# Kernel tuning notes

Hardware: AMD Instinct MI355X
Metric: run time of the kernel (lower is better)

## Reference

```python
import jax, jax.numpy as jnp
import numpy as np

D_MODEL = 2048
D_INNER = 4096            # expand * d_model
D_XB = 1024
D_STATE = 128
HEADDIM = 64
NHEADS = D_INNER // HEADDIM            # 64
NGROUPS = D_INNER // D_STATE           # 32 (d_inner == ngroups * d_state)
HPG = NHEADS // NGROUPS                # heads per B/C group = 2
REPEAT = D_INNER // D_XB               # repeat_kv factor = 4
XB_GROUPS = D_XB // D_STATE            # 8
CHUNK = 256
D_CONV = 4
CONV_DIM = D_INNER + 2 * D_XB          # 6144
D_IN_PROJ = D_INNER + 2 * D_XB + D_INNER + NHEADS  # 10304 -> d_mlp = 0
NORM_GS = D_INNER // NGROUPS           # gated group-RMSNorm group size = 128
EPS = 1e-5


def setup_inputs() -> dict:
    key = jax.random.key(0)
    ks = jax.random.split(key, 8)
    u = jax.random.normal(ks[0], (2, 2048, D_MODEL), jnp.float32)
    W_in = jax.random.normal(ks[1], (D_IN_PROJ, D_MODEL), jnp.float32) * 0.02
    conv_w = jax.random.normal(ks[2], (CONV_DIM, D_CONV), jnp.float32) * 0.2
    conv_b = jnp.zeros((CONV_DIM,), jnp.float32)
    # dt_bias = inverse-softplus of dt ~ LogUniform(dt_min, dt_max), as in __init__
    dt = jnp.exp(jax.random.uniform(ks[3], (NHEADS,), jnp.float32)
                 * (np.log(0.1) - np.log(0.001)) + np.log(0.001))
    dt_bias = dt + jnp.log(-jnp.expm1(-dt))
    A_log = jnp.log(jax.random.uniform(ks[4], (NHEADS,), jnp.float32, minval=1.0, maxval=16.0))
    D = jnp.ones((NHEADS,), jnp.float32)
    norm_weight = jnp.ones((D_INNER,), jnp.float32)
    W_out = jax.random.normal(ks[5], (D_MODEL, D_INNER), jnp.float32) * 0.02
    return dict(u=u, W_in=W_in, conv_w=conv_w, conv_b=conv_b, dt_bias=dt_bias,
                A_log=A_log, D=D, norm_weight=norm_weight, W_out=W_out)


def _segsum(x):
    # x: (..., T); out[..., t, s] = sum_{s < i <= t} x_i for s <= t else -inf
    T = x.shape[-1]
    cs = jnp.cumsum(x, axis=-1)
    seg = cs[..., :, None] - cs[..., None, :]
    mask = jnp.tril(jnp.ones((T, T), bool))
    return jnp.where(mask, seg, -jnp.inf)


def _chunked_scan(x, dt, A, Bh, Ch, D):
    # SSD chunked selective scan (mamba_chunk_scan_combined math).
    # x: (b,l,h,p), dt: (b,l,h) post-softplus, A: (h,), Bh/Ch: (b,l,h,n), D: (h,)
    b, l, h, p = x.shape
    c = l // CHUNK
    xc = x.reshape(b, c, CHUNK, h, p)
    dtc = dt.reshape(b, c, CHUNK, h)
    Bc = Bh.reshape(b, c, CHUNK, h, D_STATE)
    Cc = Ch.reshape(b, c, CHUNK, h, D_STATE)
    dA = jnp.transpose(dtc * A, (0, 3, 1, 2))          # (b,h,c,cl)
    dA_cs = jnp.cumsum(dA, axis=-1)                     # (b,h,c,cl)
    L = jnp.exp(_segsum(dA))                            # (b,h,c,cl,cl), lower-tri decay
    xdt = xc * dtc[..., None]                           # (b,c,cl,h,p)
    # intra-chunk (diagonal block) output
    G = jnp.einsum('bclhn,bcshn->bhcls', Cc, Bc)
    Y_diag = jnp.einsum('bhcls,bcshp->bclhp', G * L, xdt)
    # per-chunk final states
    decay_states = jnp.exp(dA_cs[..., -1:] - dA_cs)     # (b,h,c,cl)
    states = jnp.einsum('bcshn,bhcs,bcshp->bchpn', Bc, decay_states, xdt)
    # inter-chunk recurrence
    chunk_decay = jnp.exp(dA_cs[..., -1])               # (b,h,c)
    states_t = jnp.moveaxis(states, 1, 0)               # (c,b,h,p,n)
    decay_t = jnp.moveaxis(chunk_decay, -1, 0)          # (c,b,h)
    def step(carry, inp):
        s, d = inp
        return carry * d[..., None, None] + s, carry
    _, prev = jax.lax.scan(step, jnp.zeros_like(states_t[0]), (states_t, decay_t))
    prev = jnp.moveaxis(prev, 0, 1)                     # (b,c,h,p,n) state entering each chunk
    Y_off = jnp.einsum('bclhn,bchpn,bhcl->bclhp', Cc, prev, jnp.exp(dA_cs))
    y = Y_diag + Y_off + xc * D[:, None]                # D skip uses raw x
    return y.reshape(b, l, h, p)


def reference(u, W_in, conv_w, conv_b, dt_bias, A_log, D, norm_weight, W_out):
    b, l, _ = u.shape
    zxbcdt = u @ W_in.T                                 # (b,l,10304); d_mlp == 0
    z, xBC, dt = jnp.split(zxbcdt, [D_INNER, D_INNER + CONV_DIM], axis=-1)
    # causal depthwise conv1d (kernel D_CONV) + SiLU (causal_conv1d_fn semantics)
    xp = jnp.pad(xBC, ((0, 0), (D_CONV - 1, 0), (0, 0)))
    conv = conv_b
    for k in range(D_CONV):
        conv = conv + xp[:, k:k + l, :] * conv_w[:, k]
    xBC = jax.nn.silu(conv)
    x, B, C = jnp.split(xBC, [D_XB, 2 * D_XB], axis=-1)
    # GQA-style repeat_kv (repeat_interleave over d_state-sized groups)
    x = jnp.repeat(x.reshape(b, l, XB_GROUPS, D_STATE), REPEAT, axis=2).reshape(b, l, D_INNER)
    B = jnp.repeat(B.reshape(b, l, XB_GROUPS, D_STATE), REPEAT, axis=2)   # (b,l,NGROUPS,n)
    C = C.reshape(b, l, NGROUPS, D_STATE)
    # broadcast groups to heads (head h uses group h // HPG)
    Bh = jnp.repeat(B, HPG, axis=2)
    Ch = jnp.repeat(C, HPG, axis=2)
    xh = x.reshape(b, l, NHEADS, HEADDIM)
    dt = jax.nn.softplus(dt + dt_bias)                  # dt_softplus=True
    A = -jnp.exp(A_log)
    y = _chunked_scan(xh, dt, A, Bh, Ch, D).reshape(b, l, D_INNER)
    # RMSNormGated (norm_before_gate=False): gate then grouped RMSNorm
    y = y * jax.nn.silu(z)
    yg = y.reshape(b, l, NGROUPS, NORM_GS)
    rstd = jax.lax.rsqrt(jnp.mean(yg * yg, axis=-1, keepdims=True) + EPS)
    y = (yg * rstd).reshape(b, l, D_INNER) * norm_weight
    return y @ W_out.T
```

## Files before the change

kernel.cpp:

```cpp
#include <hip/hip_runtime.h>
#include <cstdint>
#include <cstddef>

typedef unsigned int uint;
typedef unsigned short ushort;

typedef __bf16 bf16x8 __attribute__((ext_vector_type(8)));
typedef float f32x4 __attribute__((ext_vector_type(4)));

__device__ __forceinline__ float bflo(uint u) { return __uint_as_float(u << 16); }
__device__ __forceinline__ float bfhi(uint u) { return __uint_as_float(u & 0xffff0000u); }
__device__ __forceinline__ float bf2f(ushort s) { return __uint_as_float(((uint)s) << 16); }
__device__ __forceinline__ ushort f2bf(float f) {
    uint u = __float_as_uint(f);
    u += 0x7fffu + ((u >> 16) & 1u);
    return (ushort)(u >> 16);
}
__device__ __forceinline__ uint pk2(float lo, float hi) {
    return (uint)f2bf(lo) | ((uint)f2bf(hi) << 16);
}
__device__ __forceinline__ void unpack8(uint4 v, float* f) {
    f[0] = bflo(v.x); f[1] = bfhi(v.x); f[2] = bflo(v.y); f[3] = bfhi(v.y);
    f[4] = bflo(v.z); f[5] = bfhi(v.z); f[6] = bflo(v.w); f[7] = bfhi(v.w);
}

typedef __attribute__((address_space(1))) const unsigned int* as1_cuptr;
typedef __attribute__((address_space(3))) unsigned int* as3_uptr;
__device__ __forceinline__ void gload_lds16(const void* g, void* l) {
    __builtin_amdgcn_global_load_lds((as1_cuptr)g, (as3_uptr)l, 16, 0, 0);
}

#define LTOT 4096
#define DMODEL 2048
#define DINNER 4096
#define DSTATE 128
#define NHEADS 64
#define CONVDIM 6144
#define DPROJ 10304
#define CHUNK 256
#define NCHUNK 16

__global__ void cvt_kernel(const float* __restrict__ in, ushort* __restrict__ out, int n4) {
    int i = blockIdx.x * 256 + threadIdx.x;
    if (i < n4) {
        float4 v = ((const float4*)in)[i];
        ushort4 o;
        o.x = f2bf(v.x); o.y = f2bf(v.y); o.z = f2bf(v.z); o.w = f2bf(v.w);
        ((ushort4*)out)[i] = o;
    }
}

#define MFMA_OP __builtin_amdgcn_mfma_f32_16x16x32_bf16
#define MMX(MB, AV, BV) do { \
  _Pragma("unroll") \
  for (int _m = 0; _m < 4; _m++) \
    _Pragma("unroll") \
    for (int _n = 0; _n < 4; _n++) \
      acc[(MB)+_m][_n] = MFMA_OP(AV[_m], BV[_n], acc[(MB)+_m][_n], 0, 0, 0); \
} while (0)

#define RD8(BASE, OFF) (*(const bf16x8*)((BASE) + (OFF)))

__global__ __launch_bounds__(512, 2) void gemm256_in(
    const ushort* __restrict__ X, const ushort* __restrict__ W,
    ushort* __restrict__ zbuf, ushort* __restrict__ xbc, float* __restrict__ dtraw) {
    __shared__ ushort AL[2][16384];
    __shared__ ushort BL[2][16384];
    const int NBN = 41;
    int q = gridDim.x >> 3;
    int wg = blockIdx.x;
    int swz = (wg & 7) * q + (wg >> 3);
    int per = NBN * 4;
    int sg = swz / per, rr = swz % per;
    int bm = sg * 4 + (rr & 3);
    int bn = rr >> 2;
    int tid = threadIdx.x;
    int lane = tid & 63, w = tid >> 6;
    int wr = w >> 2, wc = w & 3;
    int lr = lane & 15, g = lane >> 4;
    int y00 = ((lr >> 1) << 7) | ((lr & 1) << 6) | (g << 4);
    int z00 = y00 ^ (((y00 >> 7) & 7) << 4);
    int aBase = wr * 8192 + z00;
    int bBase = wc * 4096 + z00;
    int z0 = tid * 16, z1 = z0 + 8192;
    int y0 = z0 ^ (((z0 >> 7) & 7) << 4);
    int y1 = z1 ^ (((z1 >> 7) & 7) << 4);
    int row0s = ((y0 >> 7) << 1) | ((y0 >> 6) & 1), kbe0 = (y0 & 63) >> 1;
    int row1s = ((y1 >> 7) << 1) | ((y1 >> 6) & 1), kbe1 = (y1 & 63) >> 1;
    const ushort* gA0 = &X[(size_t)(bm * 256 + row0s) * 2048 + kbe0];
    const ushort* gA1 = &X[(size_t)(bm * 256 + row1s) * 2048 + kbe1];
    const ushort* gB0 = &W[(size_t)(bn * 256 + row0s) * 2048 + kbe0];
    const ushort* gB1 = &W[(size_t)(bn * 256 + row1s) * 2048 + kbe1];
    int wOff = w * 1024;

#define STAGE(DB, ARR, KP, P0, P1, KO) do { \
    gload_lds16((P0) + (KO) + (KP) * 32, (char*)(ARR) + (DB) * 32768 + (KP) * 16384 + wOff); \
    gload_lds16((P1) + (KO) + (KP) * 32, (char*)(ARR) + (DB) * 32768 + (KP) * 16384 + wOff + 8192); \
} while (0)

    f32x4 acc[8][4] = {};
    bf16x8 bLo[4], bHi[4], aE[4], aO[4];
    STAGE(0, AL, 0, gA0, gA1, 0);
    STAGE(0, BL, 0, gB0, gB1, 0);
    STAGE(0, AL, 1, gA0, gA1, 0);
    STAGE(0, BL, 1, gB0, gB1, 0);
    asm volatile("s_waitcnt vmcnt(4)" ::: "memory");
    __builtin_amdgcn_s_barrier();
    __builtin_amdgcn_sched_barrier(0);
    {
        const char* Ab = (const char*)AL;
        const char* Bb = (const char*)BL;
        #pragma unroll
        for (int i = 0; i < 4; i++) {
            bLo[i] = RD8(Bb, bBase + i * 1024);
            aE[i]  = RD8(Ab, aBase + i * 1024);
        }
    }

    for (int t = 0; t < 32; ++t) {
        int buf = t & 1, nb = buf ^ 1;
        int ko = ((t + 1) & 31) * 64;
        const char* Ab  = (const char*)AL + buf * 32768;
        const char* Bb  = (const char*)BL + buf * 32768;
        const char* AbN = (const char*)AL + nb * 32768;
        const char* BbN = (const char*)BL + nb * 32768;
        #pragma unroll
        for (int i = 0; i < 4; i++) aO[i] = RD8(Ab, aBase + 4096 + i * 1024);
        STAGE(nb, AL, 0, gA0, gA1, ko);
        __builtin_amdgcn_s_setprio(1);
        MMX(0, aE, bLo);
        __builtin_amdgcn_s_setprio(0);
        __builtin_amdgcn_sched_barrier(0);
        asm volatile("s_waitcnt vmcnt(2)" ::: "memory");
        __builtin_amdgcn_s_barrier();
        __builtin_amdgcn_sched_barrier(0);
        #pragma unroll
        for (int i = 0; i < 4; i++) {
            bHi[i] = RD8(Bb, bBase + 16384 + i * 1024);
            aE[i]  = RD8(Ab, aBase + 16384 + i * 1024);
        }
        STAGE(nb, BL, 0, gB0, gB1, ko);
        __builtin_amdgcn_s_setprio(1);
        MMX(4, aO, bLo);
        __builtin_amdgcn_s_setprio(0);
        __builtin_amdgcn_sched_barrier(0);
        #pragma unroll
        for (int i = 0; i < 4; i++) aO[i] = RD8(Ab, aBase + 16384 + 4096 + i * 1024);
        STAGE(nb, AL, 1, gA0, gA1, ko);
        __builtin_amdgcn_s_setprio(1);
        MMX(0, aE, bHi);
        __builtin_amdgcn_s_setprio(0);
        __builtin_amdgcn_sched_barrier(0);
        asm volatile("s_waitcnt vmcnt(2)" ::: "memory");
        __builtin_amdgcn_s_barrier();
        __builtin_amdgcn_sched_barrier(0);
        #pragma unroll
        for (int i = 0; i < 4; i++) {
            bLo[i] = RD8(BbN, bBase + i * 1024);
            aE[i]  = RD8(AbN, aBase + i * 1024);
        }
        STAGE(nb, BL, 1, gB0, gB1, ko);
        __builtin_amdgcn_s_setprio(1);
        MMX(4, aO, bHi);
        __builtin_amdgcn_s_setprio(0);
        __builtin_amdgcn_sched_barrier(0);
    }
    asm volatile("s_waitcnt vmcnt(0)" ::: "memory");

    int rq = g * 4;
    #pragma unroll
    for (int mf = 0; mf < 8; mf++) {
        int row0 = bm * 256 + wr * 128 + mf * 16 + rq;
        #pragma unroll
        for (int n = 0; n < 4; n++) {
            int cb0 = bn * 256 + wc * 64 + n * 16;
            int col = cb0 + lr;
            if (cb0 < 4096) {
                #pragma unroll
                for (int r = 0; r < 4; r++)
                    zbuf[(size_t)(row0 + r) * DINNER + col] = f2bf(acc[mf][n][r]);
            } else if (cb0 < 10240) {
                #pragma unroll
                for (int r = 0; r < 4; r++)
                    xbc[(size_t)(row0 + r) * CONVDIM + (col - 4096)] = f2bf(acc[mf][n][r]);
            } else if (cb0 < 10304) {
                #pragma unroll
                for (int r = 0; r < 4; r++)
                    dtraw[(size_t)(row0 + r) * 64 + (col - 10240)] = acc[mf][n][r];
            }
        }
    }
}
#undef STAGE

#define MM16(MB) do { \
  acc[(MB)+0][0]=MFMA_OP(a0,b0,acc[(MB)+0][0],0,0,0); acc[(MB)+0][1]=MFMA_OP(a0,b1,acc[(MB)+0][1],0,0,0); \
  acc[(MB)+0][2]=MFMA_OP(a0,b2,acc[(MB)+0][2],0,0,0); acc[(MB)+0][3]=MFMA_OP(a0,b3,acc[(MB)+0][3],0,0,0); \
  acc[(MB)+1][0]=MFMA_OP(a1,b0,acc[(MB)+1][0],0,0,0); acc[(MB)+1][1]=MFMA_OP(a1,b1,acc[(MB)+1][1],0,0,0); \
  acc[(MB)+1][2]=MFMA_OP(a1,b2,acc[(MB)+1][2],0,0,0); acc[(MB)+1][3]=MFMA_OP(a1,b3,acc[(MB)+1][3],0,0,0); \
  acc[(MB)+2][0]=MFMA_OP(a2,b0,acc[(MB)+2][0],0,0,0); acc[(MB)+2][1]=MFMA_OP(a2,b1,acc[(MB)+2][1],0,0,0); \
  acc[(MB)+2][2]=MFMA_OP(a2,b2,acc[(MB)+2][2],0,0,0); acc[(MB)+2][3]=MFMA_OP(a2,b3,acc[(MB)+2][3],0,0,0); \
  acc[(MB)+3][0]=MFMA_OP(a3,b0,acc[(MB)+3][0],0,0,0); acc[(MB)+3][1]=MFMA_OP(a3,b1,acc[(MB)+3][1],0,0,0); \
  acc[(MB)+3][2]=MFMA_OP(a3,b2,acc[(MB)+3][2],0,0,0); acc[(MB)+3][3]=MFMA_OP(a3,b3,acc[(MB)+3][3],0,0,0); \
} while (0)

__global__ __launch_bounds__(512, 2) void gemm256_out(
    const ushort* __restrict__ X, const ushort* __restrict__ W,
    float* __restrict__ outF) {
    __shared__ ushort AL[2][16384];
    __shared__ ushort BL[2][8192];
    int q = gridDim.x >> 3;
    int wg = blockIdx.x;
    int swz = (wg & 7) * q + (wg >> 3);
    int per = 16 * 4;
    int sg = swz / per, rr = swz % per;
    int bm = sg * 4 + (rr & 3);
    int bn = rr >> 2;
    int tid = threadIdx.x;
    int lane = tid & 63, w = tid >> 6;
    int wr = w >> 1, wc = w & 1;
    int lr = lane & 15, g = lane >> 4;
    int y00 = ((lr >> 1) << 7) | ((lr & 1) << 6) | (g << 4);
    int z00 = y00 ^ (((y00 >> 7) & 7) << 4);
    int aBase = wr * 4096 + z00;
    int bBase = wc * 4096 + z00;
    int z0 = tid * 16, z1 = z0 + 8192;
    int y0 = z0 ^ (((z0 >> 7) & 7) << 4);
    int y1 = z1 ^ (((z1 >> 7) & 7) << 4);
    int rowA0 = ((y0 >> 7) << 1) | ((y0 >> 6) & 1), kA0 = (y0 & 63) >> 1;
    int rowA1 = ((y1 >> 7) << 1) | ((y1 >> 6) & 1), kA1 = (y1 & 63) >> 1;
    const ushort* gA0 = &X[(size_t)(bm * 256 + rowA0) * 4096 + kA0];
    const ushort* gA1 = &X[(size_t)(bm * 256 + rowA1) * 4096 + kA1];
    const ushort* gB  = &W[(size_t)(bn * 128 + rowA0) * 4096 + kA0];
    int wOff = w * 1024;

#define STAGEA(DB, KP, KO) do { \
    gload_lds16(gA0 + (KO) + (KP) * 32, (char*)AL + (DB) * 32768 + (KP) * 16384 + wOff); \
    gload_lds16(gA1 + (KO) + (KP) * 32, (char*)AL + (DB) * 32768 + (KP) * 16384 + wOff + 8192); \
} while (0)
#define STAGEB(DB, KP, KO) \
    gload_lds16(gB + (KO) + (KP) * 32, (char*)BL + (DB) * 16384 + (KP) * 8192 + wOff)

    f32x4 acc[4][4] = {};
    STAGEA(0, 0, 0); STAGEB(0, 0, 0);
    STAGEA(0, 1, 0); STAGEB(0, 1, 0);

    for (int t = 0; t < 64; ++t) {
        int buf = t & 1, nb = buf ^ 1;
        int ko = ((t + 1) & 63) * 64;
        const char* Ab = (const char*)AL + buf * 32768;
        const char* Bb = (const char*)BL + buf * 16384;
        bf16x8 a0, a1, a2, a3, b0, b1, b2, b3;
        asm volatile("s_waitcnt vmcnt(3)" ::: "memory");
        __builtin_amdgcn_s_barrier();
        __builtin_amdgcn_sched_barrier(0);
        b0 = RD8(Bb, bBase);        b1 = RD8(Bb, bBase + 1024);
        b2 = RD8(Bb, bBase + 2048); b3 = RD8(Bb, bBase + 3072);
        a0 = RD8(Ab, aBase);        a1 = RD8(Ab, aBase + 1024);
        a2 = RD8(Ab, aBase + 2048); a3 = RD8(Ab, aBase + 3072);
        STAGEA(nb, 0, ko); STAGEB(nb, 0, ko);
        __builtin_amdgcn_s_setprio(1);
        MM16(0);
        __builtin_amdgcn_s_setprio(0);
        __builtin_amdgcn_sched_barrier(0);
        asm volatile("s_waitcnt vmcnt(3)" ::: "memory");
        __builtin_amdgcn_s_barrier();
        __builtin_amdgcn_sched_barrier(0);
        b0 = RD8(Bb, bBase + 8192);        b1 = RD8(Bb, bBase + 8192 + 1024);
        b2 = RD8(Bb, bBase + 8192 + 2048); b3 = RD8(Bb, bBase + 8192 + 3072);
        a0 = RD8(Ab, aBase + 16384);        a1 = RD8(Ab, aBase + 16384 + 1024);
        a2 = RD8(Ab, aBase + 16384 + 2048); a3 = RD8(Ab, aBase + 16384 + 3072);
        STAGEA(nb, 1, ko); STAGEB(nb, 1, ko);
        __builtin_amdgcn_s_setprio(1);
        MM16(0);
        __builtin_amdgcn_s_setprio(0);
        __builtin_amdgcn_sched_barrier(0);
    }
    asm volatile("s_waitcnt vmcnt(0)" ::: "memory");

    int rq = g * 4;
    #pragma unroll
    for (int mf = 0; mf < 4; mf++) {
        int row0 = bm * 256 + wr * 64 + mf * 16 + rq;
        #pragma unroll
        for (int nf = 0; nf < 4; nf++) {
            int col = bn * 128 + wc * 64 + nf * 16 + lr;
            #pragma unroll
            for (int r = 0; r < 4; r++)
                outF[(size_t)(row0 + r) * DMODEL + col] = acc[mf][nf][r];
        }
    }
}
#undef STAGEA
#undef STAGEB

__global__ void conv_kernel(const ushort* __restrict__ xbc, const float* __restrict__ cw,
                            const float* __restrict__ cb, ushort* __restrict__ convout) {
    int c8 = (blockIdx.x * 256 + threadIdx.x) * 8;
    int row0 = blockIdx.y * 4;
    int t0 = row0 & 2047;
    float bias[8];
    {
        float4 b0 = ((const float4*)cb)[c8 / 4];
        float4 b1 = ((const float4*)cb)[c8 / 4 + 1];
        bias[0] = b0.x; bias[1] = b0.y; bias[2] = b0.z; bias[3] = b0.w;
        bias[4] = b1.x; bias[5] = b1.y; bias[6] = b1.z; bias[7] = b1.w;
    }
    float wk[8][4];
    #pragma unroll
    for (int e = 0; e < 8; e++) {
        float4 wv = ((const float4*)cw)[c8 + e];
        wk[e][0] = wv.x; wk[e][1] = wv.y; wk[e][2] = wv.z; wk[e][3] = wv.w;
    }
    float f[7][8];
    #pragma unroll
    for (int j = 0; j < 7; j++) {
        int tt = t0 - 3 + j;
        if (tt >= 0) {
            uint4 v = *(const uint4*)&xbc[(size_t)(row0 - 3 + j) * CONVDIM + c8];
            unpack8(v, f[j]);
        } else {
            #pragma unroll
            for (int e = 0; e < 8; e++) f[j][e] = 0.f;
        }
    }
    #pragma unroll
    for (int r = 0; r < 4; r++) {
        float a[8];
        #pragma unroll
        for (int e = 0; e < 8; e++) {
            a[e] = bias[e];
            #pragma unroll
            for (int k = 0; k < 4; k++) a[e] += f[r + k][e] * wk[e][k];
        }
        uint4 o;
        float s[8];
        #pragma unroll
        for (int e = 0; e < 8; e++) s[e] = a[e] / (1.f + __expf(-a[e]));
        o.x = pk2(s[0], s[1]); o.y = pk2(s[2], s[3]);
        o.z = pk2(s[4], s[5]); o.w = pk2(s[6], s[7]);
        *(uint4*)&convout[(size_t)(row0 + r) * CONVDIM + c8] = o;
    }
}

__global__ void cumsum_kernel(float* __restrict__ dtbuf, const float* __restrict__ dt_bias,
                              const float* __restrict__ A_log, float* __restrict__ dAcs) {
    int bi = blockIdx.x;
    int h = bi & 63, cg = bi >> 6;
    int t = threadIdx.x;
    size_t didx = (size_t)(cg * 256 + t) * 64 + h;
    float x = dtbuf[didx] + dt_bias[h];
    float sp = (x > 20.f) ? x : log1pf(__expf(x));
    dtbuf[didx] = sp;
    float A = -expf(A_log[h]);
    float v = sp * A;
    __shared__ float s[256];
    s[t] = v;
    __syncthreads();
    for (int off = 1; off < 256; off <<= 1) {
        float add = (t >= off) ? s[t - off] : 0.f;
        __syncthreads();
        s[t] += add;
        __syncthreads();
    }
    dAcs[(size_t)bi * 256 + t] = s[t];
}

__global__ __launch_bounds__(256) void states_mfma(
    const ushort* __restrict__ convout, const float* __restrict__ dtsp,
    const float* __restrict__ dAcs, float* __restrict__ states) {
    __shared__ ushort BT[128 * 72];
    __shared__ ushort XT[64 * 72];
    int bi = blockIdx.x;
    int h = bi & 63, cg = bi >> 6;
    int tid = threadIdx.x;
    int rowbase = cg * 256;
    int bcol = 1024 + ((h >> 3) << 7);
    int xcol = ((h >> 3) << 7) + ((h & 1) << 6);
    float dAlast = dAcs[(size_t)bi * 256 + 255];
    int w = tid >> 6, lane = tid & 63, g = lane >> 4, cc = lane & 15;
    f32x4 acc[4][2] = {};
    for (int T = 0; T < 4; T++) {
        __syncthreads();
        int s = lane;
        int srow = rowbase + T * 64 + s;
        #pragma unroll
        for (int i = 0; i < 4; i++) {
            int n0 = (w + i * 4) * 8;
            uint4 v = *(const uint4*)&convout[(size_t)srow * CONVDIM + bcol + n0];
            ushort us[8];
            us[0] = (ushort)v.x; us[1] = (ushort)(v.x >> 16);
            us[2] = (ushort)v.y; us[3] = (ushort)(v.y >> 16);
            us[4] = (ushort)v.z; us[5] = (ushort)(v.z >> 16);
            us[6] = (ushort)v.w; us[7] = (ushort)(v.w >> 16);
            #pragma unroll
            for (int e = 0; e < 8; e++) BT[(n0 + e) * 72 + s] = us[e];
        }
        float wgt = dtsp[(size_t)srow * 64 + h] * __expf(dAlast - dAcs[(size_t)bi * 256 + T * 64 + s]);
        #pragma unroll
        for (int j = 0; j < 2; j++) {
            int p0 = (w * 2 + j) * 8;
            uint4 v = *(const uint4*)&convout[(size_t)srow * CONVDIM + xcol + p0];
            float f[8]; unpack8(v, f);
            #pragma unroll
            for (int e = 0; e < 8; e++) XT[(p0 + e) * 72 + s] = f2bf(f[e] * wgt);
        }
        __syncthreads();
        bf16x8 af[4][2], bw[2][2];
        #pragma unroll
        for (int m = 0; m < 4; m++)
            #pragma unroll
            for (int kb = 0; kb < 2; kb++)
                af[m][kb] = *(const bf16x8*)&XT[(m * 16 + cc) * 72 + kb * 32 + 8 * g];
        #pragma unroll
        for (int np = 0; np < 2; np++)
            #pragma unroll
            for (int kb = 0; kb < 2; kb++)
                bw[np][kb] = *(const bf16x8*)&BT[(w * 32 + np * 16 + cc) * 72 + kb * 32 + 8 * g];
        #pragma unroll
        for (int m = 0; m < 4; m++)
            #pragma unroll
            for (int np = 0; np < 2; np++) {
                acc[m][np] = MFMA_OP(af[m][0], bw[np][0], acc[m][np], 0, 0, 0);
                acc[m][np] = MFMA_OP(af[m][1], bw[np][1], acc[m][np], 0, 0, 0);
            }
    }
    size_t base = (size_t)bi * 8192;
    #pragma unroll
    for (int m = 0; m < 4; m++)
        #pragma unroll
        for (int np = 0; np < 2; np++)
            #pragma unroll
            for (int r = 0; r < 4; r++) {
                int p = m * 16 + 4 * g + r;
                int n = w * 32 + np * 16 + cc;
                states[base + (size_t)p * 128 + n] = acc[m][np][r];
            }
}

__global__ void recur_kernel(const float* __restrict__ dAcs, float* __restrict__ states) {
    int blk = blockIdx.x;
    int pq = blk & 7, bh = blk >> 3;
    int h = bh & 63, b = bh >> 6;
    int tid = threadIdx.x;
    int p = pq * 8 + (tid >> 5);
    int n0 = (tid & 31) * 4;
    float4 carry = make_float4(0.f, 0.f, 0.f, 0.f);
    for (int c = 0; c < 8; c++) {
        int bi = (b * 8 + c) * 64 + h;
        float decay = __expf(dAcs[(size_t)bi * 256 + 255]);
        size_t idx = (size_t)bi * 8192 + (size_t)p * 128 + n0;
        float4 tmp = *(const float4*)&states[idx];
        *(float4*)&states[idx] = carry;
        carry.x = carry.x * decay + tmp.x;
        carry.y = carry.y * decay + tmp.y;
        carry.z = carry.z * decay + tmp.z;
        carry.w = carry.w * decay + tmp.w;
    }
}

__global__ __launch_bounds__(256, 2) void yscan_mfma(
    const ushort* __restrict__ convout, const float* __restrict__ dtsp,
    const float* __restrict__ dAcs, const float* __restrict__ states,
    ushort* __restrict__ y) {
    __shared__ ushort XT[64 * 264];
    __shared__ ushort PR[64 * 136];
    __shared__ ushort PV[4 * 16 * 72];
    __shared__ float sdA[256];
    int bi = blockIdx.x;
    int h = bi & 63, cg = bi >> 6;
    int tid = threadIdx.x;
    int rowbase = cg * 256;
    int bcol = 1024 + ((h >> 3) << 7);
    int ccol = 2048 + ((h >> 1) << 7);
    int xcol = ((h >> 3) << 7) + ((h & 1) << 6);

    sdA[tid] = dAcs[(size_t)bi * 256 + tid];
    #pragma unroll
    for (int i = 0; i < 4; i++) {
        int s = i * 64 + (tid & 63);
        float dtv = dtsp[(size_t)(rowbase + s) * 64 + h];
        #pragma unroll
        for (int j = 0; j < 2; j++) {
            int p0 = (((tid >> 6) << 1) + j) << 3;
            uint4 v = *(const uint4*)&convout[(size_t)(rowbase + s) * CONVDIM + xcol + p0];
            float f[8]; unpack8(v, f);
            #pragma unroll
            for (int e = 0; e < 8; e++) XT[(p0 + e) * 264 + s] = f2bf(f[e] * dtv);
        }
    }
    {
        const float* pv = &states[(size_t)bi * 8192];
        #pragma unroll
        for (int i = 0; i < 8; i++) {
            int flat = i * 1024 + tid * 4;
            float4 v = *(const float4*)&pv[flat];
            int p = flat >> 7, n = flat & 127;
            *(uint*)&PR[p * 136 + n]     = pk2(v.x, v.y);
            *(uint*)&PR[p * 136 + n + 2] = pk2(v.z, v.w);
        }
    }
    __syncthreads();

    int w = tid >> 6, lane = tid & 63, g = lane >> 4, c = lane & 15;
    int wbase = w * 64;
    const ushort* Crow0 = &convout[(size_t)(rowbase + wbase + c) * CONVDIM + ccol + 8 * g];

    f32x4 yac[4][4] = {};
    #pragma unroll
    for (int kb = 0; kb < 4; kb++) {
        bf16x8 pb[4];
        #pragma unroll
        for (int np = 0; np < 4; np++)
            pb[np] = *(const bf16x8*)&PR[(16 * np + c) * 136 + kb * 32 + 8 * g];
        #pragma unroll
        for (int m = 0; m < 4; m++) {
            bf16x8 cf = *(const bf16x8*)&Crow0[(size_t)(m * 16) * CONVDIM + kb * 32];
            #pragma unroll
            for (int np = 0; np < 4; np++)
                yac[m][np] = MFMA_OP(cf, pb[np], yac[m][np], 0, 0, 0);
        }
    }
    float al[4][4];
    float Sw = sdA[wbase];
    float eSw = __expf(Sw);
    #pragma unroll
    for (int m = 0; m < 4; m++)
        #pragma unroll
        for (int r = 0; r < 4; r++) {
            float dAl = sdA[wbase + m * 16 + 4 * g + r];
            al[m][r] = __expf(dAl - Sw);
            float el = al[m][r] * eSw;
            #pragma unroll
            for (int np = 0; np < 4; np++) yac[m][np][r] *= el;
        }

    ushort* pvs = &PV[w * 1152];
    for (int T = 0; T <= w; T++) {
        f32x4 sac[4][4] = {};
        #pragma unroll
        for (int kb = 0; kb < 4; kb++) {
            bf16x8 bb[4];
            #pragma unroll
            for (int np = 0; np < 4; np++)
                bb[np] = *(const bf16x8*)&convout[(size_t)(rowbase + T * 64 + 16 * np + c) * CONVDIM + bcol + kb * 32 + 8 * g];
            #pragma unroll
            for (int m = 0; m < 4; m++) {
                bf16x8 cf = *(const bf16x8*)&Crow0[(size_t)(m * 16) * CONVDIM + kb * 32];
                #pragma unroll
                for (int np = 0; np < 4; np++)
                    sac[m][np] = MFMA_OP(cf, bb[np], sac[m][np], 0, 0, 0);
            }
        }
        bf16x8 xb[4][2];
        #pragma unroll
        for (int np = 0; np < 4; np++)
            #pragma unroll
            for (int k2 = 0; k2 < 2; k2++)
                xb[np][k2] = *(const bf16x8*)&XT[(16 * np + c) * 264 + T * 64 + k2 * 32 + 8 * g];
        if (T < w) {
            float ET = sdA[T * 64 + 63];
            float cT = __expf(Sw - ET);
            float bc[4];
            #pragma unroll
            for (int np = 0; np < 4; np++)
                bc[np] = __expf(ET - sdA[T * 64 + 16 * np + c]) * cT;
            #pragma unroll
            for (int m = 0; m < 4; m++) {
                #pragma unroll
                for (int np = 0; np < 4; np++) {
                    float s0 = bc[np];
                    #pragma unroll
                    for (int r = 0; r < 4; r++)
                        pvs[(4 * g + r) * 72 + 16 * np + c] = f2bf(sac[m][np][r] * (al[m][r] * s0));
                }
                bf16x8 pa0 = *(const bf16x8*)&pvs[c * 72 + 8 * g];
                bf16x8 pa1 = *(const bf16x8*)&pvs[c * 72 + 32 + 8 * g];
                #pragma unroll
                for (int np = 0; np < 4; np++) {
                    yac[m][np] = MFMA_OP(pa0, xb[np][0], yac[m][np], 0, 0, 0);
                    yac[m][np] = MFMA_OP(pa1, xb[np][1], yac[m][np], 0, 0, 0);
                }
            }
        } else {
            #pragma unroll
            for (int m = 0; m < 4; m++) {
                float dal[4];
                #pragma unroll
                for (int r = 0; r < 4; r++) dal[r] = sdA[wbase + m * 16 + 4 * g + r];
                #pragma unroll
                for (int np = 0; np < 4; np++) {
                    int s_loc = w * 64 + 16 * np + c;
                    float dAs = sdA[s_loc];
                    #pragma unroll
                    for (int r = 0; r < 4; r++) {
                        int l_loc = wbase + m * 16 + 4 * g + r;
                        float v = (s_loc <= l_loc) ? sac[m][np][r] * __expf(dal[r] - dAs) : 0.f;
                        pvs[(4 * g + r) * 72 + 16 * np + c] = f2bf(v);
                    }
                }
                bf16x8 pa0 = *(const bf16x8*)&pvs[c * 72 + 8 * g];
                bf16x8 pa1 = *(const bf16x8*)&pvs[c * 72 + 32 + 8 * g];
                #pragma unroll
                for (int np = 0; np < 4; np++) {
                    yac[m][np] = MFMA_OP(pa0, xb[np][0], yac[m][np], 0, 0, 0);
                    yac[m][np] = MFMA_OP(pa1, xb[np][1], yac[m][np], 0, 0, 0);
                }
            }
        }
    }
    #pragma unroll
    for (int m = 0; m < 4; m++)
        #pragma unroll
        for (int np = 0; np < 4; np++)
            #pragma unroll
            for (int r = 0; r < 4; r++) {
                int l = wbase + m * 16 + 4 * g + r;
                y[(size_t)(rowbase + l) * DINNER + h * 64 + 16 * np + c] = f2bf(yac[m][np][r]);
            }
}

__global__ void norm_kernel(ushort* __restrict__ y, const ushort* __restrict__ zbuf,
                            const ushort* __restrict__ convout, const float* __restrict__ Dvec,
                            const float* __restrict__ nw) {
    int row = blockIdx.x;
    int g = blockIdx.y * 4 + (threadIdx.x >> 6);
    int lane = threadIdx.x & 63;
    int cbase = g * 128 + lane * 2;
    int h = cbase >> 6;
    int p = cbase & 63;
    int xc = ((h >> 3) << 7) + ((h & 1) << 6) + p;
    uint yv = *(const uint*)&y[(size_t)row * DINNER + cbase];
    uint zv = *(const uint*)&zbuf[(size_t)row * DINNER + cbase];
    uint xv = *(const uint*)&convout[(size_t)row * CONVDIM + xc];
    float Dh = Dvec[h];
    float y0 = bflo(yv) + Dh * bflo(xv), y1 = bfhi(yv) + Dh * bfhi(xv);
    float z0 = bflo(zv), z1 = bfhi(zv);
    float v0 = y0 * (z0 / (1.f + __expf(-z0)));
    float v1 = y1 * (z1 / (1.f + __expf(-z1)));
    float ss = v0 * v0 + v1 * v1;
    #pragma unroll
    for (int off = 32; off; off >>= 1) ss += __shfl_xor(ss, off, 64);
    float rstd = rsqrtf(ss * (1.f / 128.f) + 1e-5f);
    v0 *= rstd * nw[cbase];
    v1 *= rstd * nw[cbase + 1];
    *(uint*)&y[(size_t)row * DINNER + cbase] = pk2(v0, v1);
}

extern "C" void kernel_launch(void* const* d_in, const int* in_sizes, int n_in,
                              void* d_out, int out_size, void* d_ws, size_t ws_size,
                              hipStream_t stream) {
    const float* u       = (const float*)d_in[0];
    const float* W_in    = (const float*)d_in[1];
    const float* conv_w  = (const float*)d_in[2];
    const float* conv_b  = (const float*)d_in[3];
    const float* dt_bias = (const float*)d_in[4];
    const float* A_log   = (const float*)d_in[5];
    const float* Dvec    = (const float*)d_in[6];
    const float* nw      = (const float*)d_in[7];
    const float* W_out   = (const float*)d_in[8];

    char* ws = (char*)d_ws;
    size_t off = 0;
    auto alloc = [&](size_t bytes) { void* p = ws + off; off += (bytes + 255) & ~(size_t)255; return p; };
    ushort* zbuf    = (ushort*)alloc((size_t)LTOT * DINNER * 2);
    void*   shreg   = alloc((size_t)LTOT * CONVDIM * 2);
    ushort* xbc     = (ushort*)shreg;
    float*  states  = (float*)shreg;
    ushort* Wout_bf = (ushort*)shreg;
    float*  dtbuf   = (float*) alloc((size_t)LTOT * 64 * 4);
    void*   convreg = alloc((size_t)LTOT * CONVDIM * 2);
    ushort* Win_bf  = (ushort*)convreg;
    ushort* convout = (ushort*)convreg;
    float*  dAcs    = (float*) alloc((size_t)1024 * 256 * 4);
    void*   ybreg   = alloc((size_t)LTOT * DINNER * 2);
    ushort* u_bf    = (ushort*)ybreg;
    ushort* ybuf    = (ushort*)ybreg;

    cvt_kernel<<<dim3(8192),  dim3(256), 0, stream>>>(u, u_bf, 2097152);
    cvt_kernel<<<dim3(20608), dim3(256), 0, stream>>>(W_in, Win_bf, 5275648);
    gemm256_in<<<dim3(656), dim3(512), 0, stream>>>(u_bf, Win_bf, zbuf, xbc, dtbuf);
    conv_kernel<<<dim3(3, 1024), dim3(256), 0, stream>>>(xbc, conv_w, conv_b, convout);
    cumsum_kernel<<<dim3(1024), dim3(256), 0, stream>>>(dtbuf, dt_bias, A_log, dAcs);
    states_mfma<<<dim3(1024), dim3(256), 0, stream>>>(convout, dtbuf, dAcs, states);
    recur_kernel<<<dim3(1024), dim3(256), 0, stream>>>(dAcs, states);
    yscan_mfma<<<dim3(1024), dim3(256), 0, stream>>>(convout, dtbuf, dAcs, states, ybuf);
    cvt_kernel<<<dim3(8192), dim3(256), 0, stream>>>(W_out, Wout_bf, 2097152);
    norm_kernel<<<dim3(4096, 8), dim3(256), 0, stream>>>(ybuf, zbuf, convout, Dvec, nw);
    gemm256_out<<<dim3(256), dim3(512), 0, stream>>>(ybuf, Wout_bf, (float*)d_out);
}
```

Baseline: 468.2 us.

## Triple-buffer input GEMM with 32-wide K steps and merge weight conversions

The input projection GEMM moves from double-buffered 64-wide K tiles to a three-stage ring of 32-wide K tiles. Each step now does one wait and one barrier, and loads are issued two stages ahead, so global-to-LDS latency has more time to overlap with MFMA work. LDS use drops from 128KB to 96KB per block. The three fp32-to-bf16 conversion launches are merged into one kernel, with W_out converted up front into its own new workspace buffer, which costs extra workspace memory. The GEMM now runs twice as many iterations, each with a barrier, so synchronisation overhead per unit of MFMA work goes up.

```diff
diff --git a/kernel.cpp b/kernel.cpp
--- a/kernel.cpp
+++ b/kernel.cpp
@@ -40,14 +40,19 @@
 #define CHUNK 256
 #define NCHUNK 16
 
-__global__ void cvt_kernel(const float* __restrict__ in, ushort* __restrict__ out, int n4) {
+__global__ void cvt_all(const float* __restrict__ u, const float* __restrict__ Wi,
+                        const float* __restrict__ Wo, ushort* __restrict__ ub,
+                        ushort* __restrict__ wib, ushort* __restrict__ wob) {
     int i = blockIdx.x * 256 + threadIdx.x;
-    if (i < n4) {
-        float4 v = ((const float4*)in)[i];
-        ushort4 o;
-        o.x = f2bf(v.x); o.y = f2bf(v.y); o.z = f2bf(v.z); o.w = f2bf(v.w);
-        ((ushort4*)out)[i] = o;
-    }
+    const float* src; ushort* dst; int j;
+    if (i < 2097152)      { src = u;  dst = ub;  j = i; }
+    else if (i < 7372800) { src = Wi; dst = wib; j = i - 2097152; }
+    else if (i < 9469952) { src = Wo; dst = wob; j = i - 7372800; }
+    else return;
+    float4 v = ((const float4*)src)[j];
+    ushort4 o;
+    o.x = f2bf(v.x); o.y = f2bf(v.y); o.z = f2bf(v.z); o.w = f2bf(v.w);
+    ((ushort4*)dst)[j] = o;
 }
 
 #define MFMA_OP __builtin_amdgcn_mfma_f32_16x16x32_bf16
@@ -64,8 +69,8 @@
 __global__ __launch_bounds__(512, 2) void gemm256_in(
     const ushort* __restrict__ X, const ushort* __restrict__ W,
     ushort* __restrict__ zbuf, ushort* __restrict__ xbc, float* __restrict__ dtraw) {
-    __shared__ ushort AL[2][16384];
-    __shared__ ushort BL[2][16384];
+    __shared__ ushort AL[3][8192];
+    __shared__ ushort BL[3][8192];
     const int NBN = 41;
     int q = gridDim.x >> 3;
     int wg = blockIdx.x;
@@ -93,75 +98,41 @@
     const ushort* gB1 = &W[(size_t)(bn * 256 + row1s) * 2048 + kbe1];
     int wOff = w * 1024;
 
-#define STAGE(DB, ARR, KP, P0, P1, KO) do { \
-    gload_lds16((P0) + (KO) + (KP) * 32, (char*)(ARR) + (DB) * 32768 + (KP) * 16384 + wOff); \
-    gload_lds16((P1) + (KO) + (KP) * 32, (char*)(ARR) + (DB) * 32768 + (KP) * 16384 + wOff + 8192); \
+#define STAGE(DB, ARR, P0, P1, KO) do { \
+    gload_lds16((P0) + (KO), (char*)(ARR) + (DB) * 16384 + wOff); \
+    gload_lds16((P1) + (KO), (char*)(ARR) + (DB) * 16384 + wOff + 8192); \
 } while (0)
 
     f32x4 acc[8][4] = {};
-    bf16x8 bLo[4], bHi[4], aE[4], aO[4];
-    STAGE(0, AL, 0, gA0, gA1, 0);
-    STAGE(0, BL, 0, gB0, gB1, 0);
-    STAGE(0, AL, 1, gA0, gA1, 0);
-    STAGE(0, BL, 1, gB0, gB1, 0);
-    asm volatile("s_waitcnt vmcnt(4)" ::: "memory");
-    __builtin_amdgcn_s_barrier();
-    __builtin_amdgcn_sched_barrier(0);
-    {
-        const char* Ab = (const char*)AL;
-        const char* Bb = (const char*)BL;
+    bf16x8 aE[4], aO[4], bC[4];
+    STAGE(0, AL, gA0, gA1, 0);
+    STAGE(0, BL, gB0, gB1, 0);
+    STAGE(1, AL, gA0, gA1, 32);
+    STAGE(1, BL, gB0, gB1, 32);
+
+    for (int t = 0; t < 64; ++t) {
+        int buf = t % 3, s2 = (t + 2) % 3;
+        int ko = ((t + 2) & 63) * 32;
+        const char* Ab = (const char*)AL + buf * 16384;
+        const char* Bb = (const char*)BL + buf * 16384;
+        asm volatile("s_waitcnt vmcnt(4)" ::: "memory");
+        __builtin_amdgcn_s_barrier();
+        __builtin_amdgcn_sched_barrier(0);
         #pragma unroll
         for (int i = 0; i < 4; i++) {
-            bLo[i] = RD8(Bb, bBase + i * 1024);
-            aE[i]  = RD8(Ab, aBase + i * 1024);
-        }
-    }
-
-    for (int t = 0; t < 32; ++t) {
-        int buf = t & 1, nb = buf ^ 1;
-        int ko = ((t + 1) & 31) * 64;
-        const char* Ab  = (const char*)AL + buf * 32768;
-        const char* Bb  = (const char*)BL + buf * 32768;
-        const char* AbN = (const char*)AL + nb * 32768;
-        const char* BbN = (const char*)BL + nb * 32768;
-        #pragma unroll
-        for (int i = 0; i < 4; i++) aO[i] = RD8(Ab, aBase + 4096 + i * 1024);
-        STAGE(nb, AL, 0, gA0, gA1, ko);
+            bC[i] = RD8(Bb, bBase + i * 1024);
+            aE[i] = RD8(Ab, aBase + i * 1024);
+        }
+        STAGE(s2, AL, gA0, gA1, ko);
         __builtin_amdgcn_s_setprio(1);
-        MMX(0, aE, bLo);
+        MMX(0, aE, bC);
         __builtin_amdgcn_s_setprio(0);
         __builtin_amdgcn_sched_barrier(0);
-        asm volatile("s_waitcnt vmcnt(2)" ::: "memory");
-        __builtin_amdgcn_s_barrier();
-        __builtin_amdgcn_sched_barrier(0);
-        #pragma unroll
-        for (int i = 0; i < 4; i++) {
-            bHi[i] = RD8(Bb, bBase + 16384 + i * 1024);
-            aE[i]  = RD8(Ab, aBase + 16384 + i * 1024);
-        }
-        STAGE(nb, BL, 0, gB0, gB1, ko);
+        #pragma unroll
+        for (int i = 0; i < 4; i++) aO[i] = RD8(Ab, aBase + 4096 + i * 1024);
+        STAGE(s2, BL, gB0, gB1, ko);
         __builtin_amdgcn_s_setprio(1);
-        MMX(4, aO, bLo);
-        __builtin_amdgcn_s_setprio(0);
-        __builtin_amdgcn_sched_barrier(0);
-        #pragma unroll
-        for (int i = 0; i < 4; i++) aO[i] = RD8(Ab, aBase + 16384 + 4096 + i * 1024);
-        STAGE(nb, AL, 1, gA0, gA1, ko);
-        __builtin_amdgcn_s_setprio(1);
-        MMX(0, aE, bHi);
-        __builtin_amdgcn_s_setprio(0);
-        __builtin_amdgcn_sched_barrier(0);
-        asm volatile("s_waitcnt vmcnt(2)" ::: "memory");
-        __builtin_amdgcn_s_barrier();
-        __builtin_amdgcn_sched_barrier(0);
-        #pragma unroll
-        for (int i = 0; i < 4; i++) {
-            bLo[i] = RD8(BbN, bBase + i * 1024);
-            aE[i]  = RD8(AbN, aBase + i * 1024);
-        }
-        STAGE(nb, BL, 1, gB0, gB1, ko);
-        __builtin_amdgcn_s_setprio(1);
-        MMX(4, aO, bHi);
+        MMX(4, aO, bC);
         __builtin_amdgcn_s_setprio(0);
         __builtin_amdgcn_sched_barrier(0);
     }
@@ -667,7 +638,6 @@
     void*   shreg   = alloc((size_t)LTOT * CONVDIM * 2);
     ushort* xbc     = (ushort*)shreg;
     float*  states  = (float*)shreg;
-    ushort* Wout_bf = (ushort*)shreg;
     float*  dtbuf   = (float*) alloc((size_t)LTOT * 64 * 4);
     void*   convreg = alloc((size_t)LTOT * CONVDIM * 2);
     ushort* Win_bf  = (ushort*)convreg;
@@ -676,16 +646,15 @@
     void*   ybreg   = alloc((size_t)LTOT * DINNER * 2);
     ushort* u_bf    = (ushort*)ybreg;
     ushort* ybuf    = (ushort*)ybreg;
-
-    cvt_kernel<<<dim3(8192),  dim3(256), 0, stream>>>(u, u_bf, 2097152);
-    cvt_kernel<<<dim3(20608), dim3(256), 0, stream>>>(W_in, Win_bf, 5275648);
+    ushort* Wout_bf = (ushort*)alloc((size_t)DMODEL * DINNER * 2);
+
+    cvt_all<<<dim3(36992), dim3(256), 0, stream>>>(u, W_in, W_out, u_bf, Win_bf, Wout_bf);
     gemm256_in<<<dim3(656), dim3(512), 0, stream>>>(u_bf, Win_bf, zbuf, xbc, dtbuf);
     conv_kernel<<<dim3(3, 1024), dim3(256), 0, stream>>>(xbc, conv_w, conv_b, convout);
     cumsum_kernel<<<dim3(1024), dim3(256), 0, stream>>>(dtbuf, dt_bias, A_log, dAcs);
     states_mfma<<<dim3(1024), dim3(256), 0, stream>>>(convout, dtbuf, dAcs, states);
     recur_kernel<<<dim3(1024), dim3(256), 0, stream>>>(dAcs, states);
     yscan_mfma<<<dim3(1024), dim3(256), 0, stream>>>(convout, dtbuf, dAcs, states, ybuf);
-    cvt_kernel<<<dim3(8192), dim3(256), 0, stream>>>(W_out, Wout_bf, 2097152);
     norm_kernel<<<dim3(4096, 8), dim3(256), 0, stream>>>(ybuf, zbuf, convout, Dvec, nw);
     gemm256_out<<<dim3(256), dim3(512), 0, stream>>>(ybuf, Wout_bf, (float*)d_out);
 }
```

Result: slower. 487.0 us (+4.0%).

## Merge fp32-to-bf16 conversions into one launch and software-pipeline out-proj LDS reads

Applied to the files above, without the earlier changes.

The three separate conversion kernels become a single launch that converts u, W_in and W_out in one grid. W_out's bf16 copy moves to its own workspace allocation instead of aliasing the states region, so it can be converted up front. In the output GEMM, LDS fragment reads for the next k-slice are issued before the current MFMAs, splitting each 16-MFMA block into halves placed around the barriers so reads overlap compute. This removes two launches and some LDS latency in exchange for more registers and a larger workspace.

```diff
diff --git a/kernel.cpp b/kernel.cpp
--- a/kernel.cpp
+++ b/kernel.cpp
@@ -40,14 +40,19 @@
 #define CHUNK 256
 #define NCHUNK 16
 
-__global__ void cvt_kernel(const float* __restrict__ in, ushort* __restrict__ out, int n4) {
+__global__ void cvt_all(const float* __restrict__ u, const float* __restrict__ Wi,
+                        const float* __restrict__ Wo, ushort* __restrict__ ub,
+                        ushort* __restrict__ wib, ushort* __restrict__ wob) {
     int i = blockIdx.x * 256 + threadIdx.x;
-    if (i < n4) {
-        float4 v = ((const float4*)in)[i];
-        ushort4 o;
-        o.x = f2bf(v.x); o.y = f2bf(v.y); o.z = f2bf(v.z); o.w = f2bf(v.w);
-        ((ushort4*)out)[i] = o;
-    }
+    const float* src; ushort* dst; int j;
+    if (i < 2097152)      { src = u;  dst = ub;  j = i; }
+    else if (i < 7372800) { src = Wi; dst = wib; j = i - 2097152; }
+    else if (i < 9469952) { src = Wo; dst = wob; j = i - 7372800; }
+    else return;
+    float4 v = ((const float4*)src)[j];
+    ushort4 o;
+    o.x = f2bf(v.x); o.y = f2bf(v.y); o.z = f2bf(v.z); o.w = f2bf(v.w);
+    ((ushort4*)dst)[j] = o;
 }
 
 #define MFMA_OP __builtin_amdgcn_mfma_f32_16x16x32_bf16
@@ -193,15 +198,12 @@
 }
 #undef STAGE
 
-#define MM16(MB) do { \
-  acc[(MB)+0][0]=MFMA_OP(a0,b0,acc[(MB)+0][0],0,0,0); acc[(MB)+0][1]=MFMA_OP(a0,b1,acc[(MB)+0][1],0,0,0); \
-  acc[(MB)+0][2]=MFMA_OP(a0,b2,acc[(MB)+0][2],0,0,0); acc[(MB)+0][3]=MFMA_OP(a0,b3,acc[(MB)+0][3],0,0,0); \
-  acc[(MB)+1][0]=MFMA_OP(a1,b0,acc[(MB)+1][0],0,0,0); acc[(MB)+1][1]=MFMA_OP(a1,b1,acc[(MB)+1][1],0,0,0); \
-  acc[(MB)+1][2]=MFMA_OP(a1,b2,acc[(MB)+1][2],0,0,0); acc[(MB)+1][3]=MFMA_OP(a1,b3,acc[(MB)+1][3],0,0,0); \
-  acc[(MB)+2][0]=MFMA_OP(a2,b0,acc[(MB)+2][0],0,0,0); acc[(MB)+2][1]=MFMA_OP(a2,b1,acc[(MB)+2][1],0,0,0); \
-  acc[(MB)+2][2]=MFMA_OP(a2,b2,acc[(MB)+2][2],0,0,0); acc[(MB)+2][3]=MFMA_OP(a2,b3,acc[(MB)+2][3],0,0,0); \
-  acc[(MB)+3][0]=MFMA_OP(a3,b0,acc[(MB)+3][0],0,0,0); acc[(MB)+3][1]=MFMA_OP(a3,b1,acc[(MB)+3][1],0,0,0); \
-  acc[(MB)+3][2]=MFMA_OP(a3,b2,acc[(MB)+3][2],0,0,0); acc[(MB)+3][3]=MFMA_OP(a3,b3,acc[(MB)+3][3],0,0,0); \
+#define MM8(M0, AV, BV) do { \
+  _Pragma("unroll") \
+  for (int _m = 0; _m < 2; _m++) \
+    _Pragma("unroll") \
+    for (int _n = 0; _n < 4; _n++) \
+      acc[(M0)+_m][_n] = MFMA_OP(AV[(M0)+_m], BV[_n], acc[(M0)+_m][_n], 0, 0, 0); \
 } while (0)
 
 __global__ __launch_bounds__(512, 2) void gemm256_out(
@@ -242,37 +244,54 @@
     gload_lds16(gB + (KO) + (KP) * 32, (char*)BL + (DB) * 16384 + (KP) * 8192 + wOff)
 
     f32x4 acc[4][4] = {};
+    bf16x8 aP[4], bP[4], aQ[4], bQ[4];
     STAGEA(0, 0, 0); STAGEB(0, 0, 0);
     STAGEA(0, 1, 0); STAGEB(0, 1, 0);
+    asm volatile("s_waitcnt vmcnt(3)" ::: "memory");
+    __builtin_amdgcn_s_barrier();
+    __builtin_amdgcn_sched_barrier(0);
+    #pragma unroll
+    for (int i = 0; i < 4; i++) {
+        bP[i] = RD8((const char*)BL, bBase + i * 1024);
+        aP[i] = RD8((const char*)AL, aBase + i * 1024);
+    }
 
     for (int t = 0; t < 64; ++t) {
         int buf = t & 1, nb = buf ^ 1;
         int ko = ((t + 1) & 63) * 64;
-        const char* Ab = (const char*)AL + buf * 32768;
-        const char* Bb = (const char*)BL + buf * 16384;
-        bf16x8 a0, a1, a2, a3, b0, b1, b2, b3;
+        const char* Ab  = (const char*)AL + buf * 32768;
+        const char* Bb  = (const char*)BL + buf * 16384;
+        const char* AbN = (const char*)AL + nb * 32768;
+        const char* BbN = (const char*)BL + nb * 16384;
+        STAGEA(nb, 0, ko); STAGEB(nb, 0, ko);
+        __builtin_amdgcn_s_setprio(1);
+        MM8(0, aP, bP);
+        MM8(2, aP, bP);
+        __builtin_amdgcn_s_setprio(0);
+        __builtin_amdgcn_sched_barrier(0);
         asm volatile("s_waitcnt vmcnt(3)" ::: "memory");
         __builtin_amdgcn_s_barrier();
         __builtin_amdgcn_sched_barrier(0);
-        b0 = RD8(Bb, bBase);        b1 = RD8(Bb, bBase + 1024);
-        b2 = RD8(Bb, bBase + 2048); b3 = RD8(Bb, bBase + 3072);
-        a0 = RD8(Ab, aBase);        a1 = RD8(Ab, aBase + 1024);
-        a2 = RD8(Ab, aBase + 2048); a3 = RD8(Ab, aBase + 3072);
-        STAGEA(nb, 0, ko); STAGEB(nb, 0, ko);
+        #pragma unroll
+        for (int i = 0; i < 4; i++) {
+            bQ[i] = RD8(Bb, bBase + 8192 + i * 1024);
+            aQ[i] = RD8(Ab, aBase + 16384 + i * 1024);
+        }
+        STAGEA(nb, 1, ko); STAGEB(nb, 1, ko);
         __builtin_amdgcn_s_setprio(1);
-        MM16(0);
+        MM8(0, aQ, bQ);
         __builtin_amdgcn_s_setprio(0);
         __builtin_amdgcn_sched_barrier(0);
         asm volatile("s_waitcnt vmcnt(3)" ::: "memory");
         __builtin_amdgcn_s_barrier();
         __builtin_amdgcn_sched_barrier(0);
-        b0 = RD8(Bb, bBase + 8192);        b1 = RD8(Bb, bBase + 8192 + 1024);
-        b2 = RD8(Bb, bBase + 8192 + 2048); b3 = RD8(Bb, bBase + 8192 + 3072);
-        a0 = RD8(Ab, aBase + 16384);        a1 = RD8(Ab, aBase + 16384 + 1024);
-        a2 = RD8(Ab, aBase + 16384 + 2048); a3 = RD8(Ab, aBase + 16384 + 3072);
-        STAGEA(nb, 1, ko); STAGEB(nb, 1, ko);
+        #pragma unroll
+        for (int i = 0; i < 4; i++) {
+            bP[i] = RD8(BbN, bBase + i * 1024);
+            aP[i] = RD8(AbN, aBase + i * 1024);
+        }
         __builtin_amdgcn_s_setprio(1);
-        MM16(0);
+        MM8(2, aQ, bQ);
         __builtin_amdgcn_s_setprio(0);
         __builtin_amdgcn_sched_barrier(0);
     }
@@ -667,7 +686,6 @@
     void*   shreg   = alloc((size_t)LTOT * CONVDIM * 2);
     ushort* xbc     = (ushort*)shreg;
     float*  states  = (float*)shreg;
-    ushort* Wout_bf = (ushort*)shreg;
     float*  dtbuf   = (float*) alloc((size_t)LTOT * 64 * 4);
     void*   convreg = alloc((size_t)LTOT * CONVDIM * 2);
     ushort* Win_bf  = (ushort*)convreg;
@@ -676,16 +694,15 @@
     void*   ybreg   = alloc((size_t)LTOT * DINNER * 2);
     ushort* u_bf    = (ushort*)ybreg;
     ushort* ybuf    = (ushort*)ybreg;
-
-    cvt_kernel<<<dim3(8192),  dim3(256), 0, stream>>>(u, u_bf, 2097152);
-    cvt_kernel<<<dim3(20608), dim3(256), 0, stream>>>(W_in, Win_bf, 5275648);
+    ushort* Wout_bf = (ushort*)alloc((size_t)DMODEL * DINNER * 2);
+
+    cvt_all<<<dim3(36992), dim3(256), 0, stream>>>(u, W_in, W_out, u_bf, Win_bf, Wout_bf);
     gemm256_in<<<dim3(656), dim3(512), 0, stream>>>(u_bf, Win_bf, zbuf, xbc, dtbuf);
     conv_kernel<<<dim3(3, 1024), dim3(256), 0, stream>>>(xbc, conv_w, conv_b, convout);
     cumsum_kernel<<<dim3(1024), dim3(256), 0, stream>>>(dtbuf, dt_bias, A_log, dAcs);
     states_mfma<<<dim3(1024), dim3(256), 0, stream>>>(convout, dtbuf, dAcs, states);
     recur_kernel<<<dim3(1024), dim3(256), 0, stream>>>(dAcs, states);
     yscan_mfma<<<dim3(1024), dim3(256), 0, stream>>>(convout, dtbuf, dAcs, states, ybuf);
-    cvt_kernel<<<dim3(8192), dim3(256), 0, stream>>>(W_out, Wout_bf, 2097152);
     norm_kernel<<<dim3(4096, 8), dim3(256), 0, stream>>>(ybuf, zbuf, convout, Dvec, nw);
     gemm256_out<<<dim3(256), dim3(512), 0, stream>>>(ybuf, Wout_bf, (float*)d_out);
 }
```

New measurement: 458.7 us. 1.02x faster.
